# Kernel tuning notes

Hardware: AMD Instinct MI355X
Metric: run time of the kernel (lower is better)

## Reference

```python
import jax, jax.numpy as jnp
import numpy as np

DIM = 64      # channels
HEADS = 2     # num_heads -> head_dim = 32
K = 7         # neighborhood kernel_size (hardcoded in module)
B, H, W = 1, 96, 96
STAGES = 3
HEAD_DIM = DIM // HEADS


def setup_inputs() -> dict:
    key = jax.random.key(0)
    ks = jax.random.split(key, 6)
    x = jax.random.normal(ks[0], (B, DIM, H, W), jnp.float32)
    qkv_w = jax.random.normal(ks[1], (STAGES, 3 * DIM, DIM), jnp.float32) * 0.02
    qkv_b = jnp.zeros((STAGES, 3 * DIM), jnp.float32)
    proj_w = jax.random.normal(ks[2], (STAGES, DIM, DIM), jnp.float32) * 0.02
    proj_b = jnp.zeros((STAGES, DIM), jnp.float32)
    rpb = jax.random.normal(ks[3], (STAGES, HEADS, 2 * K - 1, 2 * K - 1), jnp.float32) * 0.02
    return {"x": x, "qkv_w": qkv_w, "qkv_b": qkv_b, "proj_w": proj_w,
            "proj_b": proj_b, "rpb": rpb}


def _window_idx(n):
    # NATTEN-style clamped sliding windows: each query attends to exactly K keys.
    starts = jnp.clip(jnp.arange(n) - K // 2, 0, n - K)
    idx = starts[:, None] + jnp.arange(K)          # [n, K] absolute key positions
    rel = idx - jnp.arange(n)[:, None] + (K - 1)   # [n, K] rpb index in [0, 2K-2]
    return idx, rel


def _na_stage(x, qkv_w, qkv_b, proj_w, proj_b, rpb, prev_attn):
    # x: [B, H, W, C]
    b, h_, w_, c = x.shape
    qkv = x @ qkv_w.T + qkv_b                                    # [B,H,W,3C]
    qkv = qkv.reshape(b, h_, w_, 3, HEADS, HEAD_DIM)
    qkv = jnp.transpose(qkv, (3, 0, 4, 1, 2, 5))                 # [3,B,h,H,W,d]
    q, k, v = qkv[0], qkv[1], qkv[2]
    scale = HEAD_DIM ** -0.5

    idx_h, rel_h = _window_idx(h_)
    idx_w, rel_w = _window_idx(w_)

    def gather_nb(t):  # t: [B,h,H,W,d] -> [B,h,H,W,K*K,d]
        t = t[:, :, idx_h]                       # [B,h,H,K,W,d]
        t = t[:, :, :, :, idx_w]                 # [B,h,H,K,W,K,d]
        t = jnp.transpose(t, (0, 1, 2, 4, 3, 5, 6))  # [B,h,H,W,K,K,d]
        return t.reshape(b, HEADS, h_, w_, K * K, HEAD_DIM)

    k_nb = gather_nb(k)
    v_nb = gather_nb(v)

    attn = jnp.einsum('bhijd,bhijkd->bhijk', q * scale, k_nb)   # [B,h,H,W,K*K]

    # relative positional bias: rpb[head, rel_h, rel_w]
    bias = rpb[:, rel_h[:, :, None, None], rel_w[None, None, :, :]]  # [h,H,K,W,K]
    bias = jnp.transpose(bias, (0, 1, 3, 2, 4)).reshape(HEADS, h_, w_, K * K)
    attn = attn + bias[None]

    if prev_attn is not None:  # high-order chaining: previous attention map added to logits
        attn = attn + prev_attn

    attn = jax.nn.softmax(attn, axis=-1)
    out = jnp.einsum('bhijk,bhijkd->bhijd', attn, v_nb)          # [B,h,H,W,d]
    out = jnp.transpose(out, (0, 2, 3, 1, 4)).reshape(b, h_, w_, c)
    out = out @ proj_w.T + proj_b
    return out, attn


def reference(x, qkv_w, qkv_b, proj_w, proj_b, rpb):
    xh = jnp.transpose(x, (0, 2, 3, 1))  # NCHW -> NHWC
    attn = None
    for s in range(STAGES):
        xh, attn = _na_stage(xh, qkv_w[s], qkv_b[s], proj_w[s], proj_b[s], rpb[s], attn)
    return jnp.transpose(xh, (0, 3, 1, 2))  # NHWC -> NCHW
```

## Files before the change

### kernel.cpp

```cpp
#include <hip/hip_runtime.h>

#define HW 96
#define NPIX 9216
#define QN 192
#define ASTRIDE 52
#define SCALE 0.17677669529663687f

__device__ __forceinline__ int pmap(int bi, int bj, int px) {
    return (bi * 4 + (px >> 3)) * HW + bj * 8 + (px & 7);
}
__device__ __forceinline__ int swz(int row, int col, int sel) {
    return row * 64 + (((col & 60) ^ ((sel & 7) << 2)) | (col & 3));
}

__device__ __forceinline__ void qkv_gemm(const float* __restrict__ xs,
                                         const float* __restrict__ ws,
                                         const float* __restrict__ qb,
                                         float* __restrict__ qkv,
                                         int bi, int bj, int t)
{
    if (t >= 192) return;
    const int pxg = t & 7, jo = t >> 3;
    const int j0 = jo * 8;
    float acc[4][8];
    #pragma unroll
    for (int jj = 0; jj < 8; ++jj) {
        float bv = qb[j0 + jj];
        #pragma unroll
        for (int ii = 0; ii < 4; ++ii) acc[ii][jj] = bv;
    }
    #pragma unroll
    for (int cc = 0; cc < 16; ++cc) {
        float4 xv[4], wv[8];
        #pragma unroll
        for (int ii = 0; ii < 4; ++ii)
            xv[ii] = *(const float4*)&xs[swz(pxg * 4 + ii, cc * 4, pxg)];
        #pragma unroll
        for (int jj = 0; jj < 8; ++jj)
            wv[jj] = *(const float4*)&ws[swz(j0 + jj, cc * 4, jo)];
        #pragma unroll
        for (int ii = 0; ii < 4; ++ii)
            #pragma unroll
            for (int jj = 0; jj < 8; ++jj) {
                acc[ii][jj] = fmaf(xv[ii].x, wv[jj].x, acc[ii][jj]);
                acc[ii][jj] = fmaf(xv[ii].y, wv[jj].y, acc[ii][jj]);
                acc[ii][jj] = fmaf(xv[ii].z, wv[jj].z, acc[ii][jj]);
                acc[ii][jj] = fmaf(xv[ii].w, wv[jj].w, acc[ii][jj]);
            }
    }
    #pragma unroll
    for (int ii = 0; ii < 4; ++ii) {
        int p = pmap(bi, bj, pxg * 4 + ii);
        *(float4*)&qkv[p * QN + j0]     = make_float4(acc[ii][0], acc[ii][1], acc[ii][2], acc[ii][3]);
        *(float4*)&qkv[p * QN + j0 + 4] = make_float4(acc[ii][4], acc[ii][5], acc[ii][6], acc[ii][7]);
    }
}

template <int SRC>
__global__ __launch_bounds__(256) void k_qkv(const float* __restrict__ src,
                                             const float* __restrict__ qw,
                                             const float* __restrict__ qb,
                                             float* __restrict__ qkv)
{
    __shared__ float xs[32 * 64];
    __shared__ float ws[192 * 64];
    const int t = threadIdx.x;
    const int bi = blockIdx.x / 12, bj = blockIdx.x % 12;
    if (SRC == 0) {
        #pragma unroll
        for (int it = 0; it < 8; ++it) {
            int l = it * 256 + t;
            int c = l >> 5, px = l & 31;
            xs[swz(px, c, px >> 2)] = src[c * NPIX + pmap(bi, bj, px)];
        }
    } else {
        #pragma unroll
        for (int it = 0; it < 8; ++it) {
            int px = it * 4 + (t >> 6), c = t & 63;
            xs[swz(px, c, px >> 2)] = src[pmap(bi, bj, px) * 64 + c];
        }
    }
    #pragma unroll
    for (int it = 0; it < 12; ++it) {
        int l = it * 256 + t;
        int j = l >> 4, cs = (l & 15) * 4;
        *(float4*)&ws[swz(j, cs, j >> 3)] = *(const float4*)&qw[j * 64 + cs];
    }
    __syncthreads();
    qkv_gemm(xs, ws, qb, qkv, bi, bj, t);
}

template <int HASPREV, int LAST>
__global__ __launch_bounds__(256) void k_stage(const float* __restrict__ qkv,
                                               const float* __restrict__ rpb,
                                               const float* __restrict__ prev,
                                               float* __restrict__ cur,
                                               const float* __restrict__ pw,
                                               const float* __restrict__ pb,
                                               float* __restrict__ xh,
                                               float* __restrict__ outp)
{
    __shared__ float xs[32 * 64];
    __shared__ float ws[64 * 64];
    const int t = threadIdx.x;
    const int bi = blockIdx.x / 12, bj = blockIdx.x % 12;
    #pragma unroll
    for (int it = 0; it < 4; ++it) {
        int l = it * 256 + t;
        int j = l >> 4, cs = (l & 15) * 4;
        *(float4*)&ws[swz(j, cs, j >> 1)] = *(const float4*)&pw[j * 64 + cs];
    }
    const int r = t & 3, g = t >> 2;
    const int h = g & 1, pl = g >> 1;
    const int i = bi * 4 + (pl >> 3), jx = bj * 8 + (pl & 7);
    const int p = i * HW + jx;
    int si = i - 3;  si = si < 0 ? 0 : (si > 89 ? 89 : si);
    int sj = jx - 3; sj = sj < 0 ? 0 : (sj > 89 ? 89 : sj);
    float4 q0, q1;
    {
        const float4* qp = (const float4*)(qkv + p * QN + h * 32 + r * 8);
        q0 = qp[0]; q1 = qp[1];
        q0.x *= SCALE; q0.y *= SCALE; q0.z *= SCALE; q0.w *= SCALE;
        q1.x *= SCALE; q1.y *= SCALE; q1.z *= SCALE; q1.w *= SCALE;
    }
    const float* kb = qkv + (si * HW + sj) * QN + 64 + h * 32 + r * 8;
    float lg[49];
    #pragma unroll
    for (int a = 0; a < 7; ++a) {
        #pragma unroll
        for (int b = 0; b < 7; ++b) {
            const float4* kp = (const float4*)(kb + (a * HW + b) * QN);
            float4 k0 = kp[0], k1 = kp[1];
            float s = q0.x * k0.x;
            s = fmaf(q0.y, k0.y, s); s = fmaf(q0.z, k0.z, s); s = fmaf(q0.w, k0.w, s);
            s = fmaf(q1.x, k1.x, s); s = fmaf(q1.y, k1.y, s);
            s = fmaf(q1.z, k1.z, s); s = fmaf(q1.w, k1.w, s);
            s += __shfl_xor(s, 1);
            s += __shfl_xor(s, 2);
            lg[a * 7 + b] = s;
        }
    }
    {
        const float* rp = rpb + h * 169;
        const int rh0 = si - i + 6, rw0 = sj - jx + 6;
        #pragma unroll
        for (int a = 0; a < 7; ++a)
            #pragma unroll
            for (int b = 0; b < 7; ++b)
                lg[a * 7 + b] += rp[(rh0 + a) * 13 + rw0 + b];
    }
    if (HASPREV) {
        const float4* pp = (const float4*)(prev + (p * 2 + h) * ASTRIDE);
        #pragma unroll
        for (int k = 0; k < 12; ++k) {
            float4 z = pp[k];
            lg[k * 4]     += z.x; lg[k * 4 + 1] += z.y;
            lg[k * 4 + 2] += z.z; lg[k * 4 + 3] += z.w;
        }
        lg[48] += ((const float*)pp)[48];
    }
    float mx = lg[0];
    #pragma unroll
    for (int n = 1; n < 49; ++n) mx = fmaxf(mx, lg[n]);
    float sum = 0.f;
    #pragma unroll
    for (int n = 0; n < 49; ++n) { float e = expf(lg[n] - mx); lg[n] = e; sum += e; }
    const float inv = 1.f / sum;
    #pragma unroll
    for (int n = 0; n < 49; ++n) lg[n] *= inv;
    if (!LAST && r == 0) {
        float* cb = cur + (p * 2 + h) * ASTRIDE;
        #pragma unroll
        for (int k = 0; k < 12; ++k)
            *(float4*)&cb[k * 4] = make_float4(lg[k * 4], lg[k * 4 + 1], lg[k * 4 + 2], lg[k * 4 + 3]);
        cb[48] = lg[48];
    }
    float4 a0 = make_float4(0.f, 0.f, 0.f, 0.f), a1 = a0;
    const float* vb = kb + 64;
    #pragma unroll
    for (int a = 0; a < 7; ++a) {
        #pragma unroll
        for (int b = 0; b < 7; ++b) {
            const float4* vp = (const float4*)(vb + (a * HW + b) * QN);
            float4 v0 = vp[0], v1 = vp[1];
            const float w0 = lg[a * 7 + b];
            a0.x = fmaf(w0, v0.x, a0.x); a0.y = fmaf(w0, v0.y, a0.y);
            a0.z = fmaf(w0, v0.z, a0.z); a0.w = fmaf(w0, v0.w, a0.w);
            a1.x = fmaf(w0, v1.x, a1.x); a1.y = fmaf(w0, v1.y, a1.y);
            a1.z = fmaf(w0, v1.z, a1.z); a1.w = fmaf(w0, v1.w, a1.w);
        }
    }
    {
        const int c0 = h * 32 + r * 8;
        *(float4*)&xs[swz(pl, c0, pl >> 2)]     = a0;
        *(float4*)&xs[swz(pl, c0 + 4, pl >> 2)] = a1;
    }
    __syncthreads();
    const int pxg = t & 7, jo = t >> 3;
    const int j0 = jo * 2;
    float acc[4][2];
    {
        float b0 = pb[j0], b1 = pb[j0 + 1];
        #pragma unroll
        for (int ii = 0; ii < 4; ++ii) { acc[ii][0] = b0; acc[ii][1] = b1; }
    }
    #pragma unroll
    for (int cc = 0; cc < 16; ++cc) {
        float4 xv[4], wv[2];
        #pragma unroll
        for (int ii = 0; ii < 4; ++ii)
            xv[ii] = *(const float4*)&xs[swz(pxg * 4 + ii, cc * 4, pxg)];
        wv[0] = *(const float4*)&ws[swz(j0, cc * 4, jo)];
        wv[1] = *(const float4*)&ws[swz(j0 + 1, cc * 4, jo)];
        #pragma unroll
        for (int ii = 0; ii < 4; ++ii)
            #pragma unroll
            for (int jj = 0; jj < 2; ++jj) {
                acc[ii][jj] = fmaf(xv[ii].x, wv[jj].x, acc[ii][jj]);
                acc[ii][jj] = fmaf(xv[ii].y, wv[jj].y, acc[ii][jj]);
                acc[ii][jj] = fmaf(xv[ii].z, wv[jj].z, acc[ii][jj]);
                acc[ii][jj] = fmaf(xv[ii].w, wv[jj].w, acc[ii][jj]);
            }
    }
    if (!LAST) {
        #pragma unroll
        for (int ii = 0; ii < 4; ++ii) {
            int pg = pmap(bi, bj, pxg * 4 + ii);
            *(float2*)&xh[pg * 64 + j0] = make_float2(acc[ii][0], acc[ii][1]);
        }
    } else {
        __syncthreads();
        #pragma unroll
        for (int ii = 0; ii < 4; ++ii) {
            int px = pxg * 4 + ii;
            *(float2*)&xs[swz(px, j0, pxg)] = make_float2(acc[ii][0], acc[ii][1]);
        }
        __syncthreads();
        #pragma unroll
        for (int it = 0; it < 8; ++it) {
            int px = it * 4 + (t >> 6), c = t & 63;
            outp[c * NPIX + pmap(bi, bj, px)] = xs[swz(px, c, px >> 2)];
        }
    }
}

extern "C" void kernel_launch(void* const* d_in, const int* in_sizes, int n_in,
                              void* d_out, int out_size, void* d_ws, size_t ws_size,
                              hipStream_t stream)
{
    const float* x   = (const float*)d_in[0];
    const float* qw  = (const float*)d_in[1];
    const float* qb  = (const float*)d_in[2];
    const float* pw  = (const float*)d_in[3];
    const float* pb  = (const float*)d_in[4];
    const float* rpb = (const float*)d_in[5];
    float* out = (float*)d_out;
    float* ws  = (float*)d_ws;

    float* qkv  = ws;
    float* attA = qkv + 1769472;
    float* attB = attA + 958464;
    float* xh   = attB + 958464;

    k_qkv<0><<<288, 256, 0, stream>>>(x, qw, qb, qkv);
    k_stage<0, 0><<<288, 256, 0, stream>>>(qkv, rpb,       nullptr, attA, pw,        pb,       xh, nullptr);
    k_qkv<1><<<288, 256, 0, stream>>>(xh, qw + 12288, qb + 192, qkv);
    k_stage<1, 0><<<288, 256, 0, stream>>>(qkv, rpb + 338, attA,    attB, pw + 4096, pb + 64,  xh, nullptr);
    k_qkv<1><<<288, 256, 0, stream>>>(xh, qw + 24576, qb + 384, qkv);
    k_stage<1, 1><<<288, 256, 0, stream>>>(qkv, rpb + 676, attB, nullptr, pw + 8192, pb + 128, nullptr, out);
}
```

Measured before the change: 188.0 us.

## Fuse next-stage QKV projection into attention kernel with 6x6 tiles and ping-pong buffers

Each attention stage kernel now also computes the next stage's QKV projection from its projected output held in shared memory. This removes two separate QKV launches and the global round-trip of the intermediate activation. Tiles change from 4x8 to 6x6 pixels, giving 256 blocks of 576 threads that match the CU count. The head dimension is split across 8 lanes instead of 4, and the relative position bias is staged in shared memory. Two QKV buffers alternate so the next stage does not overwrite the neighbour data other blocks are still reading. In exchange each block loads the full QKV weight matrix again, and the shared memory footprint grows.

```diff
diff --git a/kernel.cpp b/kernel.cpp
--- a/kernel.cpp
+++ b/kernel.cpp
@@ -5,43 +5,45 @@
 #define QN 192
 #define ASTRIDE 52
 #define SCALE 0.17677669529663687f
-
-__device__ __forceinline__ int pmap(int bi, int bj, int px) {
-    return (bi * 4 + (px >> 3)) * HW + bj * 8 + (px & 7);
-}
-__device__ __forceinline__ int swz(int row, int col, int sel) {
-    return row * 64 + (((col & 60) ^ ((sel & 7) << 2)) | (col & 3));
+#define NT 576
+#define TP 36
+
+__device__ __forceinline__ int xswz(int row, int col) {
+    return row * 64 + (((col & 60) ^ (((row >> 2) & 7) << 2)) | (col & 3));
+}
+__device__ __forceinline__ int wswz(int row, int col) {
+    return row * 64 + (((col & 60) ^ ((row & 7) << 2)) | (col & 3));
 }
 
 __device__ __forceinline__ void qkv_gemm(const float* __restrict__ xs,
                                          const float* __restrict__ ws,
                                          const float* __restrict__ qb,
                                          float* __restrict__ qkv,
-                                         int bi, int bj, int t)
-{
-    if (t >= 192) return;
-    const int pxg = t & 7, jo = t >> 3;
-    const int j0 = jo * 8;
-    float acc[4][8];
-    #pragma unroll
-    for (int jj = 0; jj < 8; ++jj) {
-        float bv = qb[j0 + jj];
+                                         int i0, int j0c, int t)
+{
+    const int pxg = t % 9;
+    const int jo  = t / 9;
+    const int jb  = jo * 3;
+    float acc[4][3];
+    #pragma unroll
+    for (int jj = 0; jj < 3; ++jj) {
+        float bv = qb[jb + jj];
         #pragma unroll
         for (int ii = 0; ii < 4; ++ii) acc[ii][jj] = bv;
     }
     #pragma unroll
     for (int cc = 0; cc < 16; ++cc) {
-        float4 xv[4], wv[8];
+        float4 xv[4], wv[3];
         #pragma unroll
         for (int ii = 0; ii < 4; ++ii)
-            xv[ii] = *(const float4*)&xs[swz(pxg * 4 + ii, cc * 4, pxg)];
-        #pragma unroll
-        for (int jj = 0; jj < 8; ++jj)
-            wv[jj] = *(const float4*)&ws[swz(j0 + jj, cc * 4, jo)];
+            xv[ii] = *(const float4*)&xs[xswz(pxg * 4 + ii, cc * 4)];
+        #pragma unroll
+        for (int jj = 0; jj < 3; ++jj)
+            wv[jj] = *(const float4*)&ws[wswz(jb + jj, cc * 4)];
         #pragma unroll
         for (int ii = 0; ii < 4; ++ii)
             #pragma unroll
-            for (int jj = 0; jj < 8; ++jj) {
+            for (int jj = 0; jj < 3; ++jj) {
                 acc[ii][jj] = fmaf(xv[ii].x, wv[jj].x, acc[ii][jj]);
                 acc[ii][jj] = fmaf(xv[ii].y, wv[jj].y, acc[ii][jj]);
                 acc[ii][jj] = fmaf(xv[ii].z, wv[jj].z, acc[ii][jj]);
@@ -50,98 +52,94 @@
     }
     #pragma unroll
     for (int ii = 0; ii < 4; ++ii) {
-        int p = pmap(bi, bj, pxg * 4 + ii);
-        *(float4*)&qkv[p * QN + j0]     = make_float4(acc[ii][0], acc[ii][1], acc[ii][2], acc[ii][3]);
-        *(float4*)&qkv[p * QN + j0 + 4] = make_float4(acc[ii][4], acc[ii][5], acc[ii][6], acc[ii][7]);
-    }
-}
-
-template <int SRC>
-__global__ __launch_bounds__(256) void k_qkv(const float* __restrict__ src,
+        int px = pxg * 4 + ii;
+        float* o = qkv + ((i0 + px / 6) * HW + j0c + px % 6) * QN + jb;
+        o[0] = acc[ii][0]; o[1] = acc[ii][1]; o[2] = acc[ii][2];
+    }
+}
+
+__global__ __launch_bounds__(NT) void k_qkv0(const float* __restrict__ x,
                                              const float* __restrict__ qw,
                                              const float* __restrict__ qb,
                                              float* __restrict__ qkv)
 {
-    __shared__ float xs[32 * 64];
-    __shared__ float ws[192 * 64];
+    __shared__ float xs[TP * 64];
+    __shared__ float ws[QN * 64];
     const int t = threadIdx.x;
-    const int bi = blockIdx.x / 12, bj = blockIdx.x % 12;
-    if (SRC == 0) {
-        #pragma unroll
-        for (int it = 0; it < 8; ++it) {
-            int l = it * 256 + t;
-            int c = l >> 5, px = l & 31;
-            xs[swz(px, c, px >> 2)] = src[c * NPIX + pmap(bi, bj, px)];
-        }
-    } else {
-        #pragma unroll
-        for (int it = 0; it < 8; ++it) {
-            int px = it * 4 + (t >> 6), c = t & 63;
-            xs[swz(px, c, px >> 2)] = src[pmap(bi, bj, px) * 64 + c];
-        }
-    }
-    #pragma unroll
-    for (int it = 0; it < 12; ++it) {
-        int l = it * 256 + t;
-        int j = l >> 4, cs = (l & 15) * 4;
-        *(float4*)&ws[swz(j, cs, j >> 3)] = *(const float4*)&qw[j * 64 + cs];
-    }
-    __syncthreads();
-    qkv_gemm(xs, ws, qb, qkv, bi, bj, t);
+    const int i0 = (blockIdx.x >> 4) * 6, j0c = (blockIdx.x & 15) * 6;
+    #pragma unroll
+    for (int it = 0; it < 4; ++it) {
+        int l = it * NT + t;
+        int px = l % 36, c = l / 36;
+        xs[xswz(px, c)] = x[c * NPIX + (i0 + px / 6) * HW + j0c + px % 6];
+    }
+    #pragma unroll
+    for (int it = 0; it < 6; ++it) {
+        int l = it * NT + t;
+        if (l < 3072) {
+            int j = l >> 4, cs = (l & 15) << 2;
+            *(float4*)&ws[wswz(j, cs)] = *(const float4*)&qw[j * 64 + cs];
+        }
+    }
+    __syncthreads();
+    qkv_gemm(xs, ws, qb, qkv, i0, j0c, t);
 }
 
 template <int HASPREV, int LAST>
-__global__ __launch_bounds__(256) void k_stage(const float* __restrict__ qkv,
-                                               const float* __restrict__ rpb,
-                                               const float* __restrict__ prev,
-                                               float* __restrict__ cur,
-                                               const float* __restrict__ pw,
-                                               const float* __restrict__ pb,
-                                               float* __restrict__ xh,
-                                               float* __restrict__ outp)
-{
-    __shared__ float xs[32 * 64];
-    __shared__ float ws[64 * 64];
+__global__ __launch_bounds__(NT) void k_stage(const float* __restrict__ qkv,
+                                              const float* __restrict__ rpb,
+                                              const float* __restrict__ prev,
+                                              float* __restrict__ cur,
+                                              const float* __restrict__ pw,
+                                              const float* __restrict__ pb,
+                                              const float* __restrict__ qw,
+                                              const float* __restrict__ qb,
+                                              float* __restrict__ qkvn,
+                                              float* __restrict__ outp)
+{
+    __shared__ float xs[TP * 64];
+    __shared__ float ws[QN * 64];
+    __shared__ float rpb_s[338];
     const int t = threadIdx.x;
-    const int bi = blockIdx.x / 12, bj = blockIdx.x % 12;
-    #pragma unroll
-    for (int it = 0; it < 4; ++it) {
-        int l = it * 256 + t;
-        int j = l >> 4, cs = (l & 15) * 4;
-        *(float4*)&ws[swz(j, cs, j >> 1)] = *(const float4*)&pw[j * 64 + cs];
-    }
-    const int r = t & 3, g = t >> 2;
+    const int i0 = (blockIdx.x >> 4) * 6, j0c = (blockIdx.x & 15) * 6;
+    #pragma unroll
+    for (int it = 0; it < 2; ++it) {
+        int l = it * NT + t;
+        if (l < 1024) {
+            int j = l >> 4, cs = (l & 15) << 2;
+            *(float4*)&ws[wswz(j, cs)] = *(const float4*)&pw[j * 64 + cs];
+        }
+    }
+    if (t < 338) rpb_s[t] = rpb[t];
+    const int r = t & 7, g = t >> 3;
     const int h = g & 1, pl = g >> 1;
-    const int i = bi * 4 + (pl >> 3), jx = bj * 8 + (pl & 7);
+    const int i = i0 + pl / 6, jx = j0c + pl % 6;
     const int p = i * HW + jx;
     int si = i - 3;  si = si < 0 ? 0 : (si > 89 ? 89 : si);
     int sj = jx - 3; sj = sj < 0 ? 0 : (sj > 89 ? 89 : sj);
-    float4 q0, q1;
-    {
-        const float4* qp = (const float4*)(qkv + p * QN + h * 32 + r * 8);
-        q0 = qp[0]; q1 = qp[1];
+    float4 q0;
+    {
+        q0 = *(const float4*)(qkv + p * QN + h * 32 + r * 4);
         q0.x *= SCALE; q0.y *= SCALE; q0.z *= SCALE; q0.w *= SCALE;
-        q1.x *= SCALE; q1.y *= SCALE; q1.z *= SCALE; q1.w *= SCALE;
-    }
-    const float* kb = qkv + (si * HW + sj) * QN + 64 + h * 32 + r * 8;
+    }
+    const float* kb = qkv + (si * HW + sj) * QN + 64 + h * 32 + r * 4;
     float lg[49];
     #pragma unroll
     for (int a = 0; a < 7; ++a) {
         #pragma unroll
         for (int b = 0; b < 7; ++b) {
-            const float4* kp = (const float4*)(kb + (a * HW + b) * QN);
-            float4 k0 = kp[0], k1 = kp[1];
+            float4 k0 = *(const float4*)(kb + (a * HW + b) * QN);
             float s = q0.x * k0.x;
             s = fmaf(q0.y, k0.y, s); s = fmaf(q0.z, k0.z, s); s = fmaf(q0.w, k0.w, s);
-            s = fmaf(q1.x, k1.x, s); s = fmaf(q1.y, k1.y, s);
-            s = fmaf(q1.z, k1.z, s); s = fmaf(q1.w, k1.w, s);
             s += __shfl_xor(s, 1);
             s += __shfl_xor(s, 2);
+            s += __shfl_xor(s, 4);
             lg[a * 7 + b] = s;
         }
     }
-    {
-        const float* rp = rpb + h * 169;
+    __syncthreads();
+    {
+        const float* rp = rpb_s + h * 169;
         const int rh0 = si - i + 6, rw0 = sj - jx + 6;
         #pragma unroll
         for (int a = 0; a < 7; ++a)
@@ -175,73 +173,75 @@
             *(float4*)&cb[k * 4] = make_float4(lg[k * 4], lg[k * 4 + 1], lg[k * 4 + 2], lg[k * 4 + 3]);
         cb[48] = lg[48];
     }
-    float4 a0 = make_float4(0.f, 0.f, 0.f, 0.f), a1 = a0;
-    const float* vb = kb + 64;
-    #pragma unroll
-    for (int a = 0; a < 7; ++a) {
-        #pragma unroll
-        for (int b = 0; b < 7; ++b) {
-            const float4* vp = (const float4*)(vb + (a * HW + b) * QN);
-            float4 v0 = vp[0], v1 = vp[1];
-            const float w0 = lg[a * 7 + b];
-            a0.x = fmaf(w0, v0.x, a0.x); a0.y = fmaf(w0, v0.y, a0.y);
-            a0.z = fmaf(w0, v0.z, a0.z); a0.w = fmaf(w0, v0.w, a0.w);
-            a1.x = fmaf(w0, v1.x, a1.x); a1.y = fmaf(w0, v1.y, a1.y);
-            a1.z = fmaf(w0, v1.z, a1.z); a1.w = fmaf(w0, v1.w, a1.w);
-        }
-    }
-    {
-        const int c0 = h * 32 + r * 8;
-        *(float4*)&xs[swz(pl, c0, pl >> 2)]     = a0;
-        *(float4*)&xs[swz(pl, c0 + 4, pl >> 2)] = a1;
-    }
-    __syncthreads();
-    const int pxg = t & 7, jo = t >> 3;
-    const int j0 = jo * 2;
-    float acc[4][2];
-    {
-        float b0 = pb[j0], b1 = pb[j0 + 1];
-        #pragma unroll
-        for (int ii = 0; ii < 4; ++ii) { acc[ii][0] = b0; acc[ii][1] = b1; }
+    {
+        float4 a0 = make_float4(0.f, 0.f, 0.f, 0.f);
+        const float* vb = kb + 64;
+        #pragma unroll
+        for (int a = 0; a < 7; ++a) {
+            #pragma unroll
+            for (int b = 0; b < 7; ++b) {
+                float4 v0 = *(const float4*)(vb + (a * HW + b) * QN);
+                const float w0 = lg[a * 7 + b];
+                a0.x = fmaf(w0, v0.x, a0.x); a0.y = fmaf(w0, v0.y, a0.y);
+                a0.z = fmaf(w0, v0.z, a0.z); a0.w = fmaf(w0, v0.w, a0.w);
+            }
+        }
+        *(float4*)&xs[xswz(pl, h * 32 + r * 4)] = a0;
+    }
+    __syncthreads();
+    const int pxg = t % 18, jo = t / 18;
+    const int jb = jo * 2;
+    float pacc[2][2];
+    {
+        float b0 = pb[jb], b1 = pb[jb + 1];
+        pacc[0][0] = b0; pacc[1][0] = b0; pacc[0][1] = b1; pacc[1][1] = b1;
     }
     #pragma unroll
     for (int cc = 0; cc < 16; ++cc) {
-        float4 xv[4], wv[2];
-        #pragma unroll
-        for (int ii = 0; ii < 4; ++ii)
-            xv[ii] = *(const float4*)&xs[swz(pxg * 4 + ii, cc * 4, pxg)];
-        wv[0] = *(const float4*)&ws[swz(j0, cc * 4, jo)];
-        wv[1] = *(const float4*)&ws[swz(j0 + 1, cc * 4, jo)];
-        #pragma unroll
-        for (int ii = 0; ii < 4; ++ii)
+        float4 xv[2], wv[2];
+        #pragma unroll
+        for (int ii = 0; ii < 2; ++ii)
+            xv[ii] = *(const float4*)&xs[xswz(pxg * 2 + ii, cc * 4)];
+        #pragma unroll
+        for (int jj = 0; jj < 2; ++jj)
+            wv[jj] = *(const float4*)&ws[wswz(jb + jj, cc * 4)];
+        #pragma unroll
+        for (int ii = 0; ii < 2; ++ii)
             #pragma unroll
             for (int jj = 0; jj < 2; ++jj) {
-                acc[ii][jj] = fmaf(xv[ii].x, wv[jj].x, acc[ii][jj]);
-                acc[ii][jj] = fmaf(xv[ii].y, wv[jj].y, acc[ii][jj]);
-                acc[ii][jj] = fmaf(xv[ii].z, wv[jj].z, acc[ii][jj]);
-                acc[ii][jj] = fmaf(xv[ii].w, wv[jj].w, acc[ii][jj]);
-            }
-    }
+                pacc[ii][jj] = fmaf(xv[ii].x, wv[jj].x, pacc[ii][jj]);
+                pacc[ii][jj] = fmaf(xv[ii].y, wv[jj].y, pacc[ii][jj]);
+                pacc[ii][jj] = fmaf(xv[ii].z, wv[jj].z, pacc[ii][jj]);
+                pacc[ii][jj] = fmaf(xv[ii].w, wv[jj].w, pacc[ii][jj]);
+            }
+    }
+    __syncthreads();
+    #pragma unroll
+    for (int ii = 0; ii < 2; ++ii)
+        #pragma unroll
+        for (int jj = 0; jj < 2; ++jj)
+            xs[xswz(pxg * 2 + ii, jb + jj)] = pacc[ii][jj];
     if (!LAST) {
         #pragma unroll
-        for (int ii = 0; ii < 4; ++ii) {
-            int pg = pmap(bi, bj, pxg * 4 + ii);
-            *(float2*)&xh[pg * 64 + j0] = make_float2(acc[ii][0], acc[ii][1]);
-        }
-    } else {
-        __syncthreads();
-        #pragma unroll
-        for (int ii = 0; ii < 4; ++ii) {
-            int px = pxg * 4 + ii;
-            *(float2*)&xs[swz(px, j0, pxg)] = make_float2(acc[ii][0], acc[ii][1]);
-        }
-        __syncthreads();
-        #pragma unroll
-        for (int it = 0; it < 8; ++it) {
-            int px = it * 4 + (t >> 6), c = t & 63;
-            outp[c * NPIX + pmap(bi, bj, px)] = xs[swz(px, c, px >> 2)];
-        }
-    }
+        for (int it = 0; it < 6; ++it) {
+            int l = it * NT + t;
+            if (l < 3072) {
+                int j = l >> 4, cs = (l & 15) << 2;
+                *(float4*)&ws[wswz(j, cs)] = *(const float4*)&qw[j * 64 + cs];
+            }
+        }
+    }
+    __syncthreads();
+    if (LAST) {
+        #pragma unroll
+        for (int it = 0; it < 4; ++it) {
+            int l = it * NT + t;
+            int px = l % 36, c = l / 36;
+            outp[c * NPIX + (i0 + px / 6) * HW + j0c + px % 6] = xs[xswz(px, c)];
+        }
+        return;
+    }
+    qkv_gemm(xs, ws, qb, qkvn, i0, j0c, t);
 }
 
 extern "C" void kernel_launch(void* const* d_in, const int* in_sizes, int n_in,
@@ -257,15 +257,16 @@
     float* out = (float*)d_out;
     float* ws  = (float*)d_ws;
 
-    float* qkv  = ws;
-    float* attA = qkv + 1769472;
+    float* qkvA = ws;
+    float* qkvB = qkvA + 1769472;
+    float* attA = qkvB + 1769472;
     float* attB = attA + 958464;
-    float* xh   = attB + 958464;
-
-    k_qkv<0><<<288, 256, 0, stream>>>(x, qw, qb, qkv);
-    k_stage<0, 0><<<288, 256, 0, stream>>>(qkv, rpb,       nullptr, attA, pw,        pb,       xh, nullptr);
-    k_qkv<1><<<288, 256, 0, stream>>>(xh, qw + 12288, qb + 192, qkv);
-    k_stage<1, 0><<<288, 256, 0, stream>>>(qkv, rpb + 338, attA,    attB, pw + 4096, pb + 64,  xh, nullptr);
-    k_qkv<1><<<288, 256, 0, stream>>>(xh, qw + 24576, qb + 384, qkv);
-    k_stage<1, 1><<<288, 256, 0, stream>>>(qkv, rpb + 676, attB, nullptr, pw + 8192, pb + 128, nullptr, out);
-}
+
+    k_qkv0<<<256, NT, 0, stream>>>(x, qw, qb, qkvA);
+    k_stage<0, 0><<<256, NT, 0, stream>>>(qkvA, rpb,       nullptr, attA,
+                                          pw,        pb,       qw + 12288, qb + 192, qkvB, nullptr);
+    k_stage<1, 0><<<256, NT, 0, stream>>>(qkvB, rpb + 338, attA,    attB,
+                                          pw + 4096, pb + 64,  qw + 24576, qb + 384, qkvA, nullptr);
+    k_stage<1, 1><<<256, NT, 0, stream>>>(qkvA, rpb + 676, attB,    nullptr,
+                                          pw + 8192, pb + 128, nullptr,    nullptr,  nullptr, out);
+}
```

New measurement: 150.8 us. -19.8%, faster.
